# Kernel optimization log

Hardware: AMD Instinct MI355X
Metric: run time of the kernel (lower is better)

## Reference

```python
import jax, jax.numpy as jnp
import numpy as np

EMBED = 768
HEADS = 12
MLP_DIM = 3072
EPS = 1e-5


def _layernorm(x, g, b):
    mu = jnp.mean(x, axis=-1, keepdims=True)
    var = jnp.mean(jnp.square(x - mu), axis=-1, keepdims=True)
    return (x - mu) * jax.lax.rsqrt(var + EPS) * g + b


def setup_inputs() -> dict:
    key = jax.random.key(0)
    ks = jax.random.split(key, 8)
    B, N, C, M = 4, 1024, EMBED, MLP_DIM
    # xavier-ish scales
    x = jax.random.normal(ks[0], (B, N, C), dtype=jnp.float32)
    w_qkv = jax.random.normal(ks[1], (C, 3 * C), dtype=jnp.float32) * (2.0 / (C + 3 * C)) ** 0.5
    w_out = jax.random.normal(ks[2], (C, C), dtype=jnp.float32) * (1.0 / C) ** 0.5
    b_out = jnp.zeros((C,), dtype=jnp.float32)
    ln1_g = jnp.ones((C,), dtype=jnp.float32)
    ln1_b = jnp.zeros((C,), dtype=jnp.float32)
    ln2_g = jnp.ones((C,), dtype=jnp.float32)
    ln2_b = jnp.zeros((C,), dtype=jnp.float32)
    w1 = jax.random.normal(ks[3], (C, M), dtype=jnp.float32) * (2.0 / (C + M)) ** 0.5
    b1 = jnp.zeros((M,), dtype=jnp.float32)
    w2 = jax.random.normal(ks[4], (M, C), dtype=jnp.float32) * (2.0 / (C + M)) ** 0.5
    b2 = jnp.zeros((C,), dtype=jnp.float32)
    return {"x": x, "ln1_g": ln1_g, "ln1_b": ln1_b, "w_qkv": w_qkv, "w_out": w_out,
            "b_out": b_out, "ln2_g": ln2_g, "ln2_b": ln2_b, "w1": w1, "b1": b1,
            "w2": w2, "b2": b2}


def _block(x, ln1_g, ln1_b, w_qkv, w_out, b_out, ln2_g, ln2_b, w1, b1, w2, b2):
    B, N, C = x.shape
    H = HEADS
    D = C // H
    # ---- attention sub-block (note: original Attention adds its own residual
    # on the *normalized* input, and EncoderBlock adds x again) ----
    h = _layernorm(x, ln1_g, ln1_b)
    qkv = (h @ w_qkv).reshape(B, N, 3, H, D)
    q = qkv[:, :, 0].transpose(0, 2, 1, 3)  # [B,H,N,D]
    k = qkv[:, :, 1].transpose(0, 2, 1, 3)
    v = qkv[:, :, 2].transpose(0, 2, 1, 3)
    scores = jnp.einsum('bhnd,bhmd->bhnm', q, k) / jnp.sqrt(jnp.float32(D))
    probs = jax.nn.softmax(scores, axis=-1)
    attn = jnp.einsum('bhnm,bhmd->bhnd', probs, v)
    attn = attn.transpose(0, 2, 1, 3).reshape(B, N, C)
    attn = attn @ w_out + b_out
    x = x + (h + attn)  # double residual, faithful to source
    # ---- MLP sub-block ----
    h2 = _layernorm(x, ln2_g, ln2_b)
    h2 = jax.nn.gelu(h2 @ w1 + b1, approximate=False)
    h2 = h2 @ w2 + b2
    return x + h2


def reference(x, ln1_g, ln1_b, w_qkv, w_out, b_out, ln2_g, ln2_b, w1, b1, w2, b2):
    return _block(x, ln1_g, ln1_b, w_qkv, w_out, b_out, ln2_g, ln2_b, w1, b1, w2, b2)
```

## Files before the change

kernel.cpp:

```cpp
#include <hip/hip_runtime.h>

#define EMBED 768
#define HEADS 12
#define HDIM 64
#define MLP_DIM 3072
#define BATCH 4
#define SEQ 1024
#define ROWS (BATCH*SEQ)
#define LN_EPS 1e-5f

typedef __bf16 bf16x8 __attribute__((ext_vector_type(8)));
typedef float f32x4 __attribute__((ext_vector_type(4)));

__device__ __forceinline__ float bf2f(unsigned short h) {
    unsigned u = ((unsigned)h) << 16;
    return __builtin_bit_cast(float, u);
}
__device__ __forceinline__ unsigned short f2bf(float f) {
    unsigned u = __builtin_bit_cast(unsigned, f);
    unsigned r = (u + 0x7fffu + ((u >> 16) & 1u)) >> 16;
    return (unsigned short)r;
}

__device__ __forceinline__ void async_load16(const unsigned short* g, unsigned short* l) {
    __builtin_amdgcn_global_load_lds(
        (const __attribute__((address_space(1))) unsigned int*)g,
        (__attribute__((address_space(3))) unsigned int*)l,
        16, 0, 0);
}

__global__ void sort_vecs(const float* a0, const float* a1, const float* a2,
                          const float* a3, const float* a4, const float* a5,
                          float* g1, float* be1, float* bo,
                          float* g2, float* be2, float* bb2)
{
    const float* src[6] = {a0, a1, a2, a3, a4, a5};
    float* gdst[2] = {g1, g2};
    float* bdst[4] = {be1, bo, be2, bb2};
    float* dst[6];
    int gi = 0, bi = 0;
    for (int t = 0; t < 6; t++) {
        bool ones = (src[t][0] == 1.0f);
        if (ones) dst[t] = (gi < 2) ? gdst[gi++] : bdst[bi++];
        else      dst[t] = (bi < 4) ? bdst[bi++] : gdst[gi++];
    }
    int t = threadIdx.x;
    for (int k = 0; k < 6; k++) dst[k][t] = src[k][t];
}

__global__ void transpose_weights(const float* __restrict__ wqkv,
                                  const float* __restrict__ wout,
                                  const float* __restrict__ w1,
                                  const float* __restrict__ w2,
                                  unsigned short* __restrict__ wqkvT,
                                  unsigned short* __restrict__ woutT,
                                  unsigned short* __restrict__ w1T,
                                  unsigned short* __restrict__ w2T)
{
    __shared__ unsigned short t[32][33];
    int fb = blockIdx.x;
    const float* src; unsigned short* dst; int gx, ild, old;
    if (fb < 1728)      { src = wqkv; dst = wqkvT; gx = 72; ild = 2304; old = 768; }
    else if (fb < 2304) { fb -= 1728; src = wout; dst = woutT; gx = 24; ild = 768;  old = 768; }
    else if (fb < 4608) { fb -= 2304; src = w1;   dst = w1T;   gx = 96; ild = 3072; old = 768; }
    else                { fb -= 4608; src = w2;   dst = w2T;   gx = 24; ild = 768;  old = 3072; }
    const int j0 = (fb % gx) * 32, i0 = (fb / gx) * 32;
#pragma unroll
    for (int r = 0; r < 4; r++)
        t[threadIdx.y + r*8][threadIdx.x] =
            f2bf(src[(long)(i0 + threadIdx.y + r*8) * ild + (j0 + threadIdx.x)]);
    __syncthreads();
#pragma unroll
    for (int r = 0; r < 4; r++)
        dst[(long)(j0 + threadIdx.y + r*8) * old + (i0 + threadIdx.x)] =
            t[threadIdx.x][threadIdx.y + r*8];
}

__global__ void transpose_any(const void* __restrict__ in,
                              unsigned short* __restrict__ out,
                              int ild, int old,
                              long in_zo, long in_zi, long out_zo, long out_zi,
                              int zdiv, int in_is_f32)
{
    __shared__ unsigned short t[32][33];
    const int z = blockIdx.z;
    const long ib = (long)(z / zdiv) * in_zo  + (long)(z % zdiv) * in_zi;
    const long ob = (long)(z / zdiv) * out_zo + (long)(z % zdiv) * out_zi;
    const int j0 = blockIdx.x * 32, i0 = blockIdx.y * 32;
#pragma unroll
    for (int r = 0; r < 4; r++) {
        long idx = ib + (long)(i0 + threadIdx.y + r*8) * ild + (j0 + threadIdx.x);
        t[threadIdx.y + r*8][threadIdx.x] =
            in_is_f32 ? f2bf(((const float*)in)[idx]) : ((const unsigned short*)in)[idx];
    }
    __syncthreads();
#pragma unroll
    for (int r = 0; r < 4; r++)
        out[ob + (long)(j0 + threadIdx.y + r*8) * old + (i0 + threadIdx.x)] =
            t[threadIdx.x][threadIdx.y + r*8];
}

__global__ void ln_kernel(const float* __restrict__ xin,
                          const float* __restrict__ g,
                          const float* __restrict__ b,
                          unsigned short* __restrict__ out)
{
    const int row = blockIdx.x;
    const int tid = threadIdx.x;
    const long base = (long)row * EMBED;
    float v[3];
#pragma unroll
    for (int i = 0; i < 3; i++) v[i] = xin[base + tid + i * 256];
    float s = v[0] + v[1] + v[2];
    float s2 = v[0]*v[0] + v[1]*v[1] + v[2]*v[2];
    for (int off = 32; off; off >>= 1) { s += __shfl_down(s, off); s2 += __shfl_down(s2, off); }
    __shared__ float ps[4], ps2[4];
    int w = tid >> 6, l = tid & 63;
    if (l == 0) { ps[w] = s; ps2[w] = s2; }
    __syncthreads();
    float ts  = ps[0] + ps[1] + ps[2] + ps[3];
    float ts2 = ps2[0] + ps2[1] + ps2[2] + ps2[3];
    float mu = ts * (1.0f / EMBED);
    float var = ts2 * (1.0f / EMBED) - mu * mu;
    float rs = rsqrtf(var + LN_EPS);
#pragma unroll
    for (int i = 0; i < 3; i++) {
        int c = tid + i * 256;
        out[base + c] = f2bf((v[i] - mu) * rs * g[c] + b[c]);
    }
}

__global__ __launch_bounds__(256) void flash_attn(
    const unsigned short* __restrict__ qkv,
    const unsigned short* __restrict__ vT,
    unsigned short* __restrict__ attn)
{
    __shared__ __align__(16) unsigned short QPs[64 * 64];
    __shared__ __align__(16) unsigned short Ks[2][64 * 64];
    __shared__ __align__(16) unsigned short Vs[2][64 * 64];

    const int tid = threadIdx.x;
    const int wave = tid >> 6, lane = tid & 63;
    const int quad = lane >> 4, lr = lane & 15;
    const int q0 = blockIdx.x * 64;
    const int bh = blockIdx.y;
    const int b = bh / HEADS, h = bh % HEADS;

    const unsigned short* qb = qkv + (size_t)b * SEQ * 3 * EMBED + h * HDIM;
    const unsigned short* kb = qb + EMBED;
    const unsigned short* vb = vT + (size_t)bh * HDIM * SEQ;

#pragma unroll
    for (int cb = 0; cb < 512; cb += 256) {
        int p = cb + tid, r = p >> 3, cc = (p & 7) ^ (r & 7);
        async_load16(qb + (long)(q0 + r) * (3 * EMBED) + cc * 8, QPs + p * 8);
        async_load16(kb + (long)r * (3 * EMBED) + cc * 8, Ks[0] + p * 8);
        async_load16(vb + (long)r * SEQ + cc * 8, Vs[0] + p * 8);
    }
    __syncthreads();

    bf16x8 aq[2];
#pragma unroll
    for (int s = 0; s < 2; s++) {
        int row = wave * 16 + lr;
        aq[s] = *(const bf16x8*)&QPs[(row * 8 + ((s * 4 + quad) ^ (row & 7))) * 8];
    }

    f32x4 oacc[4];
#pragma unroll
    for (int j = 0; j < 4; j++) oacc[j] = (f32x4){0.f, 0.f, 0.f, 0.f};
    float lpart[4] = {0.f, 0.f, 0.f, 0.f};

    int cur = 0;
    for (int t = 0; t < SEQ / 64; t++) {
        bool pf = (t + 1 < SEQ / 64);
        if (pf) {
            int kv0 = (t + 1) * 64;
#pragma unroll
            for (int cb = 0; cb < 512; cb += 256) {
                int p = cb + tid, r = p >> 3, cc = (p & 7) ^ (r & 7);
                async_load16(kb + (long)(kv0 + r) * (3 * EMBED) + cc * 8, Ks[cur ^ 1] + p * 8);
                async_load16(vb + (long)r * SEQ + kv0 + cc * 8, Vs[cur ^ 1] + p * 8);
            }
        }
        f32x4 sacc[4];
#pragma unroll
        for (int j = 0; j < 4; j++) sacc[j] = (f32x4){0.f, 0.f, 0.f, 0.f};
#pragma unroll
        for (int s = 0; s < 2; s++)
#pragma unroll
            for (int j = 0; j < 4; j++) {
                int row = j * 16 + lr;
                bf16x8 bk = *(const bf16x8*)&Ks[cur][(row * 8 + ((s * 4 + quad) ^ (lr & 7))) * 8];
                sacc[j] = __builtin_amdgcn_mfma_f32_16x16x32_bf16(aq[s], bk, sacc[j], 0, 0, 0);
            }
#pragma unroll
        for (int j = 0; j < 4; j++)
#pragma unroll
            for (int r = 0; r < 4; r++) {
                float e = __expf(sacc[j][r] * 0.125f);
                lpart[r] += e;
                int row = wave * 16 + quad * 4 + r;
                int cc = (2 * j + (lr >> 3)) ^ (row & 7);
                QPs[(row * 8 + cc) * 8 + (lr & 7)] = f2bf(e);
            }
#pragma unroll
        for (int s = 0; s < 2; s++) {
            int prow = wave * 16 + lr;
            bf16x8 ap = *(const bf16x8*)&QPs[(prow * 8 + ((s * 4 + quad) ^ (prow & 7))) * 8];
#pragma unroll
            for (int j = 0; j < 4; j++) {
                int vrow = j * 16 + lr;
                bf16x8 bv = *(const bf16x8*)&Vs[cur][(vrow * 8 + ((s * 4 + quad) ^ (lr & 7))) * 8];
                oacc[j] = __builtin_amdgcn_mfma_f32_16x16x32_bf16(ap, bv, oacc[j], 0, 0, 0);
            }
        }
        __syncthreads();
        cur ^= 1;
    }
#pragma unroll
    for (int off = 1; off < 16; off <<= 1)
#pragma unroll
        for (int r = 0; r < 4; r++) lpart[r] += __shfl_xor(lpart[r], off);
#pragma unroll
    for (int j = 0; j < 4; j++)
#pragma unroll
        for (int r = 0; r < 4; r++) {
            int row = q0 + wave * 16 + quad * 4 + r;
            attn[(size_t)(b * SEQ + row) * EMBED + h * HDIM + j * 16 + lr] =
                f2bf(oacc[j][r] / lpart[r]);
        }
}

__global__ __launch_bounds__(512) void gemm_bt0(
    const unsigned short* __restrict__ A, int lda,
    const unsigned short* __restrict__ Bt, int ldb,
    int Kdim,
    const float* __restrict__ bias,
    unsigned short* __restrict__ Cb,
    int ldc, int gelu_flag)
{
    constexpr int BK = 32;
    __shared__ __align__(16) unsigned short As[2][128 * BK];
    __shared__ __align__(16) unsigned short Bs[2][128 * BK];

    const int tid = threadIdx.x;
    const int wave = tid >> 6;
    const int lane = tid & 63;
    const int quad = lane >> 4;
    const int lrow = lane & 15;
    const int wr = wave >> 2;
    const int wc = wave & 3;

    int bx = blockIdx.x, by = blockIdx.y;
    {
        int flat = by * gridDim.x + bx;
        int xcd = flat & 7, seq = flat >> 3;
        int ypg = gridDim.y >> 3;
        by = xcd * ypg + seq / gridDim.x;
        bx = seq % gridDim.x;
    }
    const int m0 = by * 128;
    const int n0 = bx * 128;

    f32x4 acc[4][2];
#pragma unroll
    for (int i = 0; i < 4; i++)
#pragma unroll
        for (int j = 0; j < 2; j++) acc[i][j] = (f32x4){0.f, 0.f, 0.f, 0.f};

    const int srow = tid >> 2;
    const int scol = (tid & 3) * 8;

    auto stage = [&](int k0, int bsel) {
        async_load16(A  + (long)(m0 + srow) * lda + k0 + scol,
                     (unsigned short*)As[bsel] + tid * 8);
        async_load16(Bt + (long)(n0 + srow) * ldb + k0 + scol,
                     (unsigned short*)Bs[bsel] + tid * 8);
    };

    stage(0, 0);
    __syncthreads();
    int cur = 0;

    for (int k0 = 0; k0 < Kdim; k0 += BK) {
        if (k0 + BK < Kdim) stage(k0 + BK, cur ^ 1);

        bf16x8 af[4], bfv[2];
#pragma unroll
        for (int i = 0; i < 4; i++)
            af[i] = *reinterpret_cast<const bf16x8*>(
                &As[cur][(wr*64 + i*16 + lrow) * BK + quad * 8]);
#pragma unroll
        for (int j = 0; j < 2; j++)
            bfv[j] = *reinterpret_cast<const bf16x8*>(
                &Bs[cur][(wc*32 + j*16 + lrow) * BK + quad * 8]);
#pragma unroll
        for (int i = 0; i < 4; i++)
#pragma unroll
            for (int j = 0; j < 2; j++)
                acc[i][j] = __builtin_amdgcn_mfma_f32_16x16x32_bf16(
                    af[i], bfv[j], acc[i][j], 0, 0, 0);

        __syncthreads();
        cur ^= 1;
    }

#pragma unroll
    for (int i = 0; i < 4; i++)
#pragma unroll
        for (int j = 0; j < 2; j++)
#pragma unroll
            for (int r = 0; r < 4; r++) {
                int row = m0 + wr*64 + i*16 + quad*4 + r;
                int col = n0 + wc*32 + j*16 + lrow;
                float v = acc[i][j][r];
                if (bias) v += bias[col];
                if (gelu_flag) v = 0.5f * v * (1.0f + erff(v * 0.70710678118654752f));
                Cb[(long)row * ldc + col] = f2bf(v);
            }
}

__global__ __launch_bounds__(512) void gemm_bt64(
    const unsigned short* __restrict__ A, int lda,
    const unsigned short* __restrict__ Bt, int ldb,
    int Kdim,
    const float* __restrict__ bias,
    const unsigned short* __restrict__ res1,
    const float* __restrict__ resf,
    float* __restrict__ Cf,
    unsigned short* __restrict__ Cb,
    int ldc)
{
    __shared__ __align__(16) unsigned short As[2][64 * 64];
    __shared__ __align__(16) unsigned short Bs[2][64 * 64];

    const int tid = threadIdx.x;
    const int wave = tid >> 6;
    const int lane = tid & 63;
    const int quad = lane >> 4;
    const int lr = lane & 15;
    const int wr = wave >> 1;
    const int sw = wave & 1;

    int bx = blockIdx.x, by = blockIdx.y;
    {
        int flat = by * gridDim.x + bx;
        int xcd = flat & 7, seq = flat >> 3;
        int ypg = gridDim.y >> 3;
        by = xcd * ypg + seq / gridDim.x;
        bx = seq % gridDim.x;
    }
    const int m0 = by * 64;
    const int n0 = bx * 64;

    f32x4 acc[4];
#pragma unroll
    for (int j = 0; j < 4; j++) acc[j] = (f32x4){0.f, 0.f, 0.f, 0.f};

    auto stage = [&](int k0, unsigned short* Ad, unsigned short* Bd) {
        int p = tid, r = p >> 3, cc = (p & 7) ^ (r & 7);
        async_load16(A + (long)(m0 + r) * lda + k0 + cc * 8, Ad + p * 8);
        async_load16(Bt + (long)(n0 + r) * ldb + k0 + cc * 8, Bd + p * 8);
    };

    stage(0, As[0], Bs[0]);
    __syncthreads();
    int cur = 0;

    for (int k0 = 0; k0 < Kdim; k0 += 64) {
        if (k0 + 64 < Kdim) stage(k0 + 64, As[cur ^ 1], Bs[cur ^ 1]);

        int arow = wr * 16 + lr;
        bf16x8 af = *(const bf16x8*)&As[cur][(arow * 8 + ((sw * 4 + quad) ^ (lr & 7))) * 8];
#pragma unroll
        for (int j = 0; j < 4; j++) {
            int brow = j * 16 + lr;
            bf16x8 bv = *(const bf16x8*)&Bs[cur][(brow * 8 + ((sw * 4 + quad) ^ (lr & 7))) * 8];
            acc[j] = __builtin_amdgcn_mfma_f32_16x16x32_bf16(af, bv, acc[j], 0, 0, 0);
        }
        __syncthreads();
        cur ^= 1;
    }

    float* mbuf = (float*)As;
    if (sw == 1) {
#pragma unroll
        for (int j = 0; j < 4; j++)
#pragma unroll
            for (int r = 0; r < 4; r++)
                mbuf[(wr * 16 + quad * 4 + r) * 64 + j * 16 + lr] = acc[j][r];
    }
    __syncthreads();
    if (sw == 0) {
#pragma unroll
        for (int j = 0; j < 4; j++)
#pragma unroll
            for (int r = 0; r < 4; r++) {
                int lrow_o = wr * 16 + quad * 4 + r;
                int row = m0 + lrow_o;
                int col = n0 + j * 16 + lr;
                float v = acc[j][r] + mbuf[lrow_o * 64 + j * 16 + lr];
                if (bias) v += bias[col];
                long idx = (long)row * ldc + col;
                if (res1) v += bf2f(res1[idx]);
                if (resf) v += resf[idx];
                if (Cf) Cf[idx] = v;
                else    Cb[idx] = f2bf(v);
            }
    }
}

extern "C" void kernel_launch(void* const* d_in, const int* in_sizes, int n_in,
                              void* d_out, int out_size, void* d_ws, size_t ws_size,
                              hipStream_t stream)
{
    int ix = -1, iwqkv = -1, iwout = -1, iw1 = -1, iw2 = -1, ib1 = -1;
    int v768[8]; int nv = 0;
    for (int i = 0; i < n_in; i++) {
        int s = in_sizes[i];
        if      (s == ROWS*EMBED)        ix = i;
        else if (s == EMBED*3*EMBED)     iwqkv = i;
        else if (s == EMBED*EMBED)       iwout = i;
        else if (s == EMBED*MLP_DIM)     { if (iw1 < 0) iw1 = i; else iw2 = i; }
        else if (s == MLP_DIM)           ib1 = i;
        else if (s == EMBED && nv < 8)   v768[nv++] = i;
    }
    if (n_in != 12 || ix < 0 || iwqkv < 0 || iwout < 0 || iw1 < 0 || iw2 < 0 ||
        ib1 < 0 || nv != 6)
        return;

    const float* x    = (const float*)d_in[ix];
    const float* wqkv = (const float*)d_in[iwqkv];
    const float* wout = (const float*)d_in[iwout];
    const float* w1   = (const float*)d_in[iw1];
    const float* w2   = (const float*)d_in[iw2];
    const float* b1   = (const float*)d_in[ib1];
    float* out = (float*)d_out;

    char* ws = (char*)d_ws;
    size_t off = 0;
    auto alloc = [&](size_t bytes) -> char* {
        char* p = ws + off;
        off += (bytes + 255) & ~(size_t)255;
        return p;
    };
    unsigned short* h_bf  = (unsigned short*)alloc((size_t)ROWS * EMBED * 2);
    unsigned short* qkv   = (unsigned short*)alloc((size_t)ROWS * 3 * EMBED * 2);
    unsigned short* vT    = (unsigned short*)alloc((size_t)BATCH * HEADS * HDIM * SEQ * 2);
    unsigned short* attn  = (unsigned short*)alloc((size_t)ROWS * EMBED * 2);
    float*          x2f   = (float*)alloc((size_t)ROWS * EMBED * 4);
    unsigned short* wqkvT = (unsigned short*)alloc((size_t)3 * EMBED * EMBED * 2);
    unsigned short* woutT = (unsigned short*)alloc((size_t)EMBED * EMBED * 2);
    unsigned short* w1T   = (unsigned short*)alloc((size_t)MLP_DIM * EMBED * 2);
    unsigned short* w2T   = (unsigned short*)alloc((size_t)EMBED * MLP_DIM * 2);
    unsigned short* h2    = (unsigned short*)alloc((size_t)ROWS * EMBED * 2);
    float* vecs           = (float*)alloc((size_t)(6 * EMBED) * 4);
    if (off > ws_size) return;

    float* ln1g_f = vecs;
    float* ln1b_f = vecs + EMBED;
    float* bout_f = vecs + 2 * EMBED;
    float* ln2g_f = vecs + 3 * EMBED;
    float* ln2b_f = vecs + 4 * EMBED;
    float* b2_f   = vecs + 5 * EMBED;
    unsigned short* u = qkv;

    sort_vecs<<<1, 768, 0, stream>>>(
        (const float*)d_in[v768[0]], (const float*)d_in[v768[1]],
        (const float*)d_in[v768[2]], (const float*)d_in[v768[3]],
        (const float*)d_in[v768[4]], (const float*)d_in[v768[5]],
        ln1g_f, ln1b_f, bout_f, ln2g_f, ln2b_f, b2_f);

    dim3 tb(32, 8);
    transpose_weights<<<6912, tb, 0, stream>>>(wqkv, wout, w1, w2,
                                               wqkvT, woutT, w1T, w2T);

    ln_kernel<<<ROWS, 256, 0, stream>>>(x, ln1g_f, ln1b_f, h_bf);

    gemm_bt0<<<dim3(3*EMBED/128, ROWS/128), 512, 0, stream>>>(
        h_bf, EMBED, wqkvT, EMBED, EMBED, nullptr, qkv, 3*EMBED, 0);

    transpose_any<<<dim3(HDIM/32, SEQ/32, BATCH*HEADS), tb, 0, stream>>>(
        qkv + 2*EMBED, vT, 3*EMBED, SEQ,
        (long)SEQ*3*EMBED, (long)HDIM,
        (long)HEADS*HDIM*SEQ, (long)HDIM*SEQ, HEADS, 0);

    flash_attn<<<dim3(SEQ/64, BATCH*HEADS), 256, 0, stream>>>(qkv, vT, attn);

    gemm_bt64<<<dim3(EMBED/64, ROWS/64), 512, 0, stream>>>(
        attn, EMBED, woutT, EMBED, EMBED,
        bout_f, h_bf, x, x2f, nullptr, EMBED);

    ln_kernel<<<ROWS, 256, 0, stream>>>(x2f, ln2g_f, ln2b_f, h2);

    gemm_bt0<<<dim3(MLP_DIM/128, ROWS/128), 512, 0, stream>>>(
        h2, EMBED, w1T, EMBED, EMBED, b1, u, MLP_DIM, 1);

    gemm_bt64<<<dim3(EMBED/64, ROWS/64), 512, 0, stream>>>(
        u, MLP_DIM, w2T, MLP_DIM, MLP_DIM,
        b2_f, nullptr, x2f, out, nullptr, EMBED);
}
```

Baseline: 273.7 us.

## Triple-buffer GEMM LDS staging with vmcnt-based waits and swizzled layout

Both bf16 GEMM kernels move from double to triple buffering in LDS, prefetching two K-tiles ahead. The full __syncthreads is replaced with a partial s_waitcnt vmcnt plus a raw barrier, so loads for the next tiles stay in flight while the current tile is consumed. The 128x128 kernel also gets an XOR swizzle on the LDS column index to reduce bank conflicts on fragment reads. This raises LDS use per block, which may lower occupancy, and correctness now depends on the hand-written vmcnt counts matching the issued async loads.

```diff
diff --git a/kernel.cpp b/kernel.cpp
--- a/kernel.cpp
+++ b/kernel.cpp
@@ -28,6 +28,10 @@
         (__attribute__((address_space(3))) unsigned int*)l,
         16, 0, 0);
 }
+
+#define WAIT_VMCNT(N) asm volatile("s_waitcnt vmcnt(" #N ")" ::: "memory")
+#define RAW_BARRIER() do { __builtin_amdgcn_s_barrier(); \
+                           asm volatile("" ::: "memory"); } while (0)
 
 __global__ void sort_vecs(const float* a0, const float* a1, const float* a2,
                           const float* a3, const float* a4, const float* a5,
@@ -241,8 +245,8 @@
     int ldc, int gelu_flag)
 {
     constexpr int BK = 32;
-    __shared__ __align__(16) unsigned short As[2][128 * BK];
-    __shared__ __align__(16) unsigned short Bs[2][128 * BK];
+    __shared__ __align__(16) unsigned short As[3][128 * BK];
+    __shared__ __align__(16) unsigned short Bs[3][128 * BK];
 
     const int tid = threadIdx.x;
     const int wave = tid >> 6;
@@ -270,31 +274,42 @@
         for (int j = 0; j < 2; j++) acc[i][j] = (f32x4){0.f, 0.f, 0.f, 0.f};
 
     const int srow = tid >> 2;
-    const int scol = (tid & 3) * 8;
+    const int sccp = (tid & 3) ^ ((tid >> 4) & 3);
+    const unsigned short* aSrc = A  + (long)(m0 + srow) * lda + sccp * 8;
+    const unsigned short* bSrc = Bt + (long)(n0 + srow) * ldb + sccp * 8;
 
     auto stage = [&](int k0, int bsel) {
-        async_load16(A  + (long)(m0 + srow) * lda + k0 + scol,
-                     (unsigned short*)As[bsel] + tid * 8);
-        async_load16(Bt + (long)(n0 + srow) * ldb + k0 + scol,
-                     (unsigned short*)Bs[bsel] + tid * 8);
+        async_load16(aSrc + k0, (unsigned short*)As[bsel] + tid * 8);
+        async_load16(bSrc + k0, (unsigned short*)Bs[bsel] + tid * 8);
     };
 
+    const int NT = Kdim / BK;
     stage(0, 0);
-    __syncthreads();
+    stage(BK, 1);
+    WAIT_VMCNT(2);
+    RAW_BARRIER();
+
+    const int xr = (lrow >> 2) & 3;
     int cur = 0;
-
-    for (int k0 = 0; k0 < Kdim; k0 += BK) {
-        if (k0 + BK < Kdim) stage(k0 + BK, cur ^ 1);
+    for (int t = 0; t < NT; t++) {
+        if (t + 2 < NT) {
+            int s2 = cur + 2; if (s2 >= 3) s2 -= 3;
+            stage((t + 2) * BK, s2);
+        }
 
         bf16x8 af[4], bfv[2];
 #pragma unroll
-        for (int i = 0; i < 4; i++)
+        for (int i = 0; i < 4; i++) {
+            int row = wr*64 + i*16 + lrow;
             af[i] = *reinterpret_cast<const bf16x8*>(
-                &As[cur][(wr*64 + i*16 + lrow) * BK + quad * 8]);
-#pragma unroll
-        for (int j = 0; j < 2; j++)
+                &As[cur][(row * 4 + (quad ^ xr)) * 8]);
+        }
+#pragma unroll
+        for (int j = 0; j < 2; j++) {
+            int row = wc*32 + j*16 + lrow;
             bfv[j] = *reinterpret_cast<const bf16x8*>(
-                &Bs[cur][(wc*32 + j*16 + lrow) * BK + quad * 8]);
+                &Bs[cur][(row * 4 + (quad ^ xr)) * 8]);
+        }
 #pragma unroll
         for (int i = 0; i < 4; i++)
 #pragma unroll
@@ -302,8 +317,10 @@
                 acc[i][j] = __builtin_amdgcn_mfma_f32_16x16x32_bf16(
                     af[i], bfv[j], acc[i][j], 0, 0, 0);
 
-        __syncthreads();
-        cur ^= 1;
+        if (t + 2 < NT) WAIT_VMCNT(2);
+        else            WAIT_VMCNT(0);
+        RAW_BARRIER();
+        cur = cur + 1; if (cur >= 3) cur -= 3;
     }
 
 #pragma unroll
@@ -332,8 +349,8 @@
     unsigned short* __restrict__ Cb,
     int ldc)
 {
-    __shared__ __align__(16) unsigned short As[2][64 * 64];
-    __shared__ __align__(16) unsigned short Bs[2][64 * 64];
+    __shared__ __align__(16) unsigned short As[3][64 * 64];
+    __shared__ __align__(16) unsigned short Bs[3][64 * 64];
 
     const int tid = threadIdx.x;
     const int wave = tid >> 6;
@@ -358,18 +375,28 @@
 #pragma unroll
     for (int j = 0; j < 4; j++) acc[j] = (f32x4){0.f, 0.f, 0.f, 0.f};
 
-    auto stage = [&](int k0, unsigned short* Ad, unsigned short* Bd) {
-        int p = tid, r = p >> 3, cc = (p & 7) ^ (r & 7);
-        async_load16(A + (long)(m0 + r) * lda + k0 + cc * 8, Ad + p * 8);
-        async_load16(Bt + (long)(n0 + r) * ldb + k0 + cc * 8, Bd + p * 8);
+    const int sr = tid >> 3;
+    const int scc = (tid & 7) ^ (sr & 7);
+    const unsigned short* aSrc = A  + (long)(m0 + sr) * lda + scc * 8;
+    const unsigned short* bSrc = Bt + (long)(n0 + sr) * ldb + scc * 8;
+
+    auto stage = [&](int k0, int bsel) {
+        async_load16(aSrc + k0, As[bsel] + tid * 8);
+        async_load16(bSrc + k0, Bs[bsel] + tid * 8);
     };
 
-    stage(0, As[0], Bs[0]);
-    __syncthreads();
+    const int NT = Kdim / 64;
+    stage(0, 0);
+    stage(64, 1);
+    WAIT_VMCNT(2);
+    RAW_BARRIER();
+
     int cur = 0;
-
-    for (int k0 = 0; k0 < Kdim; k0 += 64) {
-        if (k0 + 64 < Kdim) stage(k0 + 64, As[cur ^ 1], Bs[cur ^ 1]);
+    for (int t = 0; t < NT; t++) {
+        if (t + 2 < NT) {
+            int s2 = cur + 2; if (s2 >= 3) s2 -= 3;
+            stage((t + 2) * 64, s2);
+        }
 
         int arow = wr * 16 + lr;
         bf16x8 af = *(const bf16x8*)&As[cur][(arow * 8 + ((sw * 4 + quad) ^ (lr & 7))) * 8];
@@ -379,8 +406,11 @@
             bf16x8 bv = *(const bf16x8*)&Bs[cur][(brow * 8 + ((sw * 4 + quad) ^ (lr & 7))) * 8];
             acc[j] = __builtin_amdgcn_mfma_f32_16x16x32_bf16(af, bv, acc[j], 0, 0, 0);
         }
-        __syncthreads();
-        cur ^= 1;
+
+        if (t + 2 < NT) WAIT_VMCNT(2);
+        else            WAIT_VMCNT(0);
+        RAW_BARRIER();
+        cur = cur + 1; if (cur >= 3) cur -= 3;
     }
 
     float* mbuf = (float*)As;
```

Result: no change. 277.8 us (+1.5%).
